# Kernel tuning notes

Hardware: AMD Instinct MI355X
Metric: run time of the kernel (lower is better)

Reference implementation:

```python
import jax, jax.numpy as jnp
from jax import lax
import numpy as np

MS = 128            # local_map_size
HALF = MS // 2
B, S = 8, 64
C, H, W = 3, 1024, 1024


def setup_inputs() -> dict:
    key = jax.random.key(0)
    ks = jax.random.split(key, 48)
    r = lambda i, shape, s: jax.random.normal(ks[i], shape, jnp.float32) * s
    z = lambda *shape: jnp.zeros(shape, jnp.float32)
    o = lambda *shape: jnp.ones(shape, jnp.float32)
    return {
        "full_map": jax.random.normal(ks[0], (B, C, H, W), jnp.float32),
        "conditions": jax.random.uniform(ks[1], (B, 5), jnp.float32, 0.0, 1024.0),
        "input_seq": jax.random.uniform(ks[2], (B, S, 2), jnp.float32, 0.0, 1024.0),
        "steps_remaining": jax.random.uniform(ks[3], (B, S), jnp.float32, 0.0, 500.0),
        # LocalMapEncoder convs (OIHW) + batchnorm affine params
        "cw1": r(4, (16, 3, 3, 3), 0.2),   "cb1": z(16),  "g1": o(16),  "be1": z(16),
        "cw2": r(5, (32, 16, 3, 3), 0.1),  "cb2": z(32),  "g2": o(32),  "be2": z(32),
        "cw3": r(6, (64, 32, 3, 3), 0.07), "cb3": z(64),  "g3": o(64),  "be3": z(64),
        "cw4": r(7, (128, 64, 3, 3), 0.05),"cb4": z(128), "g4": o(128), "be4": z(128),
        "fw1": r(8, (512, 128 * 8 * 8), 0.01), "fb1": z(512),
        "fw2": r(9, (256, 512), 0.04),         "fb2": z(256),
        # ConditionEncoder (6 -> 128 -> 64)
        "ew1": r(10, (128, 6), 0.05),  "eb1": z(128),
        "ew2": r(11, (64, 128), 0.05), "eb2": z(64),
        # coord embedder (2 -> 32)
        "mw": r(12, (32, 2), 0.05), "mb": z(32),
        # 2-layer LSTM, torch gate order (i, f, g, o)
        "w_ih0": r(13, (4 * 256, 32), 0.05),  "w_hh0": r(14, (4 * 256, 256), 0.05),
        "b_ih0": z(4 * 256), "b_hh0": z(4 * 256),
        "w_ih1": r(15, (4 * 256, 256), 0.05), "w_hh1": r(16, (4 * 256, 256), 0.05),
        "b_ih1": z(4 * 256), "b_hh1": z(4 * 256),
        # context layer (256+256+64=576 -> 128 -> 64) and output (64 -> 2)
        "xw1": r(17, (128, 576), 0.04), "xb1": z(128),
        "xw2": r(18, (64, 128), 0.05),  "xb2": z(64),
        "ow": r(19, (2, 64), 0.1),      "ob": z(2),
    }


def _conv_bn_relu(x, w, b, g, be):
    # stride-2 3x3 conv, padding 1, NCHW/OIHW; BatchNorm in training mode (batch stats)
    y = lax.conv_general_dilated(x, w, (2, 2), ((1, 1), (1, 1)),
                                 dimension_numbers=("NCHW", "OIHW", "NCHW"))
    y = y + b[None, :, None, None]
    mu = y.mean((0, 2, 3), keepdims=True)
    var = y.var((0, 2, 3), keepdims=True)
    y = (y - mu) * lax.rsqrt(var + 1e-5) * g[None, :, None, None] + be[None, :, None, None]
    return jax.nn.relu(y)


def _lstm_layer(x, w_ih, w_hh, b_ih, b_hh):
    # x: [B, S, D] -> hidden states [B, S, Hd]
    bsz, hd = x.shape[0], w_hh.shape[1]
    bias = b_ih + b_hh
    def step(carry, xt):
        h, c = carry
        zg = xt @ w_ih.T + h @ w_hh.T + bias
        i, f, gg, oo = jnp.split(zg, 4, axis=-1)
        c = jax.nn.sigmoid(f) * c + jax.nn.sigmoid(i) * jnp.tanh(gg)
        h = jax.nn.sigmoid(oo) * jnp.tanh(c)
        return (h, c), h
    h0 = jnp.zeros((bsz, hd), x.dtype)
    _, hs = lax.scan(step, (h0, h0), x.transpose(1, 0, 2))
    return hs.transpose(1, 0, 2)


def reference(full_map, conditions, input_seq, steps_remaining,
              cw1, cb1, g1, be1, cw2, cb2, g2, be2,
              cw3, cb3, g3, be3, cw4, cb4, g4, be4,
              fw1, fb1, fw2, fb2, ew1, eb1, ew2, eb2, mw, mb,
              w_ih0, w_hh0, b_ih0, b_hh0, w_ih1, w_hh1, b_ih1, b_hh1,
              xw1, xb1, xw2, xb2, ow, ob):
    bsz, seq, _ = input_seq.shape
    # --- batched crop+pad gather (replaces host numpy loop): zero-pad map by
    # HALF on each side, then every crop is a dynamic_slice of size MS at (y, x).
    padded = jnp.pad(full_map, ((0, 0), (0, 0), (HALF, HALF), (HALF, HALF)))
    ys = input_seq[..., 0].astype(jnp.int32).reshape(-1)
    xs = input_seq[..., 1].astype(jnp.int32).reshape(-1)
    bidx = jnp.repeat(jnp.arange(bsz, dtype=jnp.int32), seq)
    crop_one = lambda b, y, x: lax.dynamic_slice(padded, (b, 0, y, x), (1, C, MS, MS))[0]
    crops = jax.vmap(crop_one)(bidx, ys, xs)              # [B*S, C, MS, MS]
    # --- LocalMapEncoder
    h = _conv_bn_relu(crops, cw1, cb1, g1, be1)
    h = _conv_bn_relu(h, cw2, cb2, g2, be2)
    h = _conv_bn_relu(h, cw3, cb3, g3, be3)
    h = _conv_bn_relu(h, cw4, cb4, g4, be4)               # [B*S, 128, 8, 8]
    h = h.reshape(h.shape[0], -1)
    h = jax.nn.relu(h @ fw1.T + fb1) @ fw2.T + fb2
    map_features = h.reshape(bsz, seq, -1)                # [B, S, 256]
    # --- ConditionEncoder on [conditions ++ steps_remaining]
    enh = jnp.concatenate(
        [jnp.broadcast_to(conditions[:, None, :], (bsz, seq, 5)),
         steps_remaining[..., None]], axis=-1)            # [B, S, 6]
    cond_features = jax.nn.relu(enh @ ew1.T + eb1) @ ew2.T + eb2  # [B, S, 64]
    # --- route predictor
    emb = jax.nn.relu(input_seq @ mw.T + mb)              # [B, S, 32]
    lstm_out = _lstm_layer(emb, w_ih0, w_hh0, b_ih0, b_hh0)
    lstm_out = _lstm_layer(lstm_out, w_ih1, w_hh1, b_ih1, b_hh1)  # [B, S, 256]
    combined = jnp.concatenate([lstm_out, map_features, cond_features], axis=-1)
    ctx = jax.nn.relu(jax.nn.relu(combined @ xw1.T + xb1) @ xw2.T + xb2)
    return ctx @ ow.T + ob                                # [B, S, 2]
```

## Files before the change

### kernel.cpp

```cpp
#include <hip/hip_runtime.h>

#define TPB 256
#define NLB 64

typedef float f32x4 __attribute__((ext_vector_type(4)));
typedef short bf16x8 __attribute__((ext_vector_type(8)));
typedef unsigned long long u64;

__device__ __forceinline__ float bf2f(unsigned short u) {
  union { unsigned int i; float f; } x; x.i = ((unsigned int)u) << 16; return x.f;
}
__device__ __forceinline__ unsigned short f2bf(float v) {
  union { float f; unsigned int i; } x; x.f = v;
  unsigned int r = (x.i + 0x7fffu + ((x.i >> 16) & 1u)) >> 16;
  return (unsigned short)r;
}
__device__ __forceinline__ float sigf(float x) { return 1.f / (1.f + __expf(-x)); }
__device__ __forceinline__ bf16x8 lda_bf8(const unsigned short* p) {
  union { uint4 u; bf16x8 v; } t; t.u = *(const uint4*)p; return t.v;
}
__device__ __forceinline__ bf16x8 frag_of(const unsigned int* w) {
  union { unsigned int u[4]; bf16x8 v; } t;
  t.u[0] = w[0]; t.u[1] = w[1]; t.u[2] = w[2]; t.u[3] = w[3]; return t.v;
}

__global__ __launch_bounds__(TPB, 2) void conv1_tap(
    const float* __restrict__ fmap, const float* __restrict__ iseq,
    const unsigned short* __restrict__ wT,
    const float* __restrict__ bias,
    unsigned short* __restrict__ out, float* __restrict__ part) {
  __shared__ __align__(16) unsigned short patch[17][132][8];
  __shared__ unsigned short Bsm[16][104];
  __shared__ float bs[16];
  __shared__ float swsum[4][16], swsq[4][16];
  const int tid = threadIdx.x;
  const int n = blockIdx.x >> 3, R0 = (blockIdx.x & 7) << 3;
  const int y = (int)iseq[n * 2], x = (int)iseq[n * 2 + 1];
  const int bimg = n >> 6;

  for (int e = tid; e < 1536; e += TPB) Bsm[e / 96][e % 96] = wT[e];
  if (tid < 16) bs[tid] = bias[tid];
  for (int e = tid; e < 17 * 132; e += TPB)
    *(uint4*)&patch[e / 132][e % 132][0] = uint4{0u, 0u, 0u, 0u};
  __syncthreads();
  for (int e = tid; e < 3 * 17 * 132; e += TPB) {
    int ic = e / 2244, rem = e % 2244, l = rem / 132, c = rem % 132;
    int i = 2 * R0 - 1 + l, j = c - 1;
    float v = 0.f;
    if ((unsigned)i < 128u && (unsigned)j < 128u) {
      int r = y + i - 64, cc = x + j - 64;
      if ((unsigned)r < 1024u && (unsigned)cc < 1024u)
        v = fmap[(((size_t)bimg * 3 + ic) << 20) + ((size_t)r << 10) + cc];
    }
    patch[l][c][ic] = f2bf(v);
  }
  __syncthreads();

  const int w = tid >> 6, lane = tid & 63, fr = lane & 15, kg = lane >> 4;
  f32x4 acc[8];
#pragma unroll
  for (int m = 0; m < 8; ++m) acc[m] = {0.f, 0.f, 0.f, 0.f};

#pragma unroll
  for (int ch = 0; ch < 3; ++ch) {
    int k8 = ch * 4 + kg;
    int ki = (k8 >= 9) ? 0 : ((k8 * 11) >> 5);
    int kj = (k8 >= 9) ? 0 : (k8 - 3 * ki);
    bf16x8 bfr = lda_bf8(&Bsm[fr][k8 * 8]);
#pragma unroll
    for (int m = 0; m < 8; ++m) {
      int p = w * 128 + m * 16 + fr;
      int pr = p >> 6, pc = p & 63;
      bf16x8 af = lda_bf8(&patch[2 * pr + ki][2 * pc + kj][0]);
      acc[m] = __builtin_amdgcn_mfma_f32_16x16x32_bf16(af, bfr, acc[m], 0, 0, 0);
    }
  }
  const int rg = lane >> 4;
  float bb = bs[fr];
  float sps = 0.f, spq = 0.f;
#pragma unroll
  for (int m = 0; m < 8; ++m) {
#pragma unroll
    for (int r = 0; r < 4; ++r) {
      int p = w * 128 + m * 16 + rg * 4 + r;
      int pr = p >> 6, pc = p & 63;
      float v = acc[m][r] + bb;
      sps += v; spq = fmaf(v, v, spq);
      out[(((size_t)n * 64 + R0 + pr) * 64 + pc) * 16 + fr] = f2bf(v);
    }
  }
  sps += __shfl_xor(sps, 16); spq += __shfl_xor(spq, 16);
  sps += __shfl_xor(sps, 32); spq += __shfl_xor(spq, 32);
  if (lane < 16) { swsum[w][fr] = sps; swsq[w][fr] = spq; }
  __syncthreads();
  if (tid < 16) {
    float s = swsum[0][tid] + swsum[1][tid] + swsum[2][tid] + swsum[3][tid];
    float q = swsq[0][tid] + swsq[1][tid] + swsq[2][tid] + swsq[3][tid];
    part[(size_t)blockIdx.x * 32 + tid * 2] = s;
    part[(size_t)blockIdx.x * 32 + tid * 2 + 1] = q;
  }
}

template<int CIN, int COUT_BLK, int NSPLIT, int HIN, int HOUT>
__global__ __launch_bounds__(TPB, 2) void conv_tap(
    const unsigned short* __restrict__ inb,
    const float* __restrict__ ss,
    const unsigned short* __restrict__ wT,
    const float* __restrict__ bias,
    unsigned short* __restrict__ out, float* __restrict__ part) {
  constexpr int K = CIN * 9;
  constexpr int K8 = K / 8;
  constexpr int NCH = (K8 + 3) / 4;
  constexpr int KPAD = NCH * 32;
  constexpr int BS = KPAD + 8;
  constexpr int CINP = CIN + 8;
  constexpr int ICG_SH = (CIN == 16) ? 1 : (CIN == 32) ? 2 : 3;
  constexpr int TPR = HOUT / 8;
  constexpr int TILES = TPR * TPR;
  constexpr int NT = COUT_BLK / 16;
  constexpr int COUT_TOT = COUT_BLK * NSPLIT;

  __shared__ unsigned short patch[289 * CINP];
  __shared__ unsigned short Bsm[COUT_BLK * BS];
  __shared__ float ssl[CIN * 2];
  __shared__ float swsum[4][COUT_BLK], swsq[4][COUT_BLK];

  const int tid = threadIdx.x;
  const int bid = blockIdx.x;
  const int n = bid / (TILES * NSPLIT);
  const int rem = bid % (TILES * NSPLIT);
  const int tile = rem / NSPLIT;
  const int split = rem % NSPLIT;
  const int TR0 = (tile / TPR) * 8, TC0 = (tile % TPR) * 8;
  const int oc0 = split * COUT_BLK;

  for (int i = tid; i < CIN * 2; i += TPB) ssl[i] = ss[i];
  __syncthreads();

  for (int e = tid; e < 289 * (CIN / 8); e += TPB) {
    int icg = e % (CIN / 8), pix = e / (CIN / 8);
    int row = pix / 17, col = pix % 17;
    int ir = 2 * TR0 - 1 + row, jc = 2 * TC0 - 1 + col;
    uint4 o = {0u, 0u, 0u, 0u};
    if ((unsigned)ir < (unsigned)HIN && (unsigned)jc < (unsigned)HIN) {
      uint4 v = *(const uint4*)&inb[(((size_t)n * HIN + ir) * HIN + jc) * CIN + icg * 8];
      unsigned int d[4] = {v.x, v.y, v.z, v.w};
      unsigned int* op = (unsigned int*)&o;
#pragma unroll
      for (int t = 0; t < 4; ++t) {
        int c = icg * 8 + 2 * t;
        float a = fmaxf(fmaf(bf2f((unsigned short)(d[t] & 0xffff)), ssl[2 * c], ssl[2 * c + 1]), 0.f);
        float b = fmaxf(fmaf(bf2f((unsigned short)(d[t] >> 16)), ssl[2 * c + 2], ssl[2 * c + 3]), 0.f);
        op[t] = (unsigned int)f2bf(a) | ((unsigned int)f2bf(b) << 16);
      }
    }
    *(uint4*)&patch[pix * CINP + icg * 8] = o;
  }
  constexpr int B8 = COUT_BLK * (KPAD / 8);
  for (int e = tid; e < B8; e += TPB) {
    int oc = e / (KPAD / 8), k8i = e % (KPAD / 8);
    uint4 v = {0u, 0u, 0u, 0u};
    if (k8i * 8 < K) v = *(const uint4*)&wT[(size_t)(oc0 + oc) * K + k8i * 8];
    *(uint4*)&Bsm[oc * BS + k8i * 8] = v;
  }
  __syncthreads();

  const int wave = tid >> 6, lane = tid & 63;
  const int fr = lane & 15, kg = lane >> 4;
  const int p = wave * 16 + fr;
  const int pr = p >> 3, pc = p & 7;
  f32x4 acc[NT];
#pragma unroll
  for (int j = 0; j < NT; ++j) acc[j] = {0.f, 0.f, 0.f, 0.f};

#pragma unroll
  for (int ch = 0; ch < NCH; ++ch) {
    int k8 = ch * 4 + kg;
    int tap = k8 >> ICG_SH, icg = k8 & ((1 << ICG_SH) - 1);
    int ki = (tap * 11) >> 5;
    int kj = tap - 3 * ki;
    int addr = ((2 * pr + ki) * 17 + (2 * pc + kj)) * CINP + icg * 8;
    if (tap >= 9) addr = 0;
    bf16x8 af = lda_bf8(&patch[addr]);
#pragma unroll
    for (int j = 0; j < NT; ++j) {
      bf16x8 bfr = lda_bf8(&Bsm[(j * 16 + fr) * BS + ch * 32 + kg * 8]);
      acc[j] = __builtin_amdgcn_mfma_f32_16x16x32_bf16(af, bfr, acc[j], 0, 0, 0);
    }
  }
  const int rg = lane >> 4;
#pragma unroll
  for (int j = 0; j < NT; ++j) {
    int oc = oc0 + j * 16 + fr;
    float bb = bias[oc];
    float s1 = 0.f, q1 = 0.f;
#pragma unroll
    for (int r = 0; r < 4; ++r) {
      int pp = wave * 16 + rg * 4 + r;
      int orow = TR0 + (pp >> 3), ocol = TC0 + (pp & 7);
      float v = acc[j][r] + bb;
      s1 += v; q1 = fmaf(v, v, q1);
      out[(((size_t)n * HOUT + orow) * HOUT + ocol) * COUT_TOT + oc] = f2bf(v);
    }
    s1 += __shfl_xor(s1, 16); q1 += __shfl_xor(q1, 16);
    s1 += __shfl_xor(s1, 32); q1 += __shfl_xor(q1, 32);
    if (lane < 16) { swsum[wave][j * 16 + fr] = s1; swsq[wave][j * 16 + fr] = q1; }
  }
  __syncthreads();
  if (tid < COUT_BLK) {
    float s = swsum[0][tid] + swsum[1][tid] + swsum[2][tid] + swsum[3][tid];
    float q = swsq[0][tid] + swsq[1][tid] + swsq[2][tid] + swsq[3][tid];
    part[(size_t)bid * COUT_BLK * 2 + tid * 2] = s;
    part[(size_t)bid * COUT_BLK * 2 + tid * 2 + 1] = q;
  }
}

__global__ __launch_bounds__(TPB) void stats_final3(const float* __restrict__ part,
    const float* __restrict__ gamma, const float* __restrict__ beta,
    float* __restrict__ ss, float inv_count, int COUT_BLK, int NSPLIT, int NBID) {
  const int c = blockIdx.x, tid = threadIdx.x;
  const int split = c / COUT_BLK, loc = c % COUT_BLK;
  const int NG = NBID / NSPLIT;
  float s = 0.f, q = 0.f;
  for (int g = tid; g < NG; g += TPB) {
    size_t b = (size_t)g * NSPLIT + split;
    s += part[b * COUT_BLK * 2 + loc * 2];
    q += part[b * COUT_BLK * 2 + loc * 2 + 1];
  }
  __shared__ float rs[TPB], rq[TPB];
  rs[tid] = s; rq[tid] = q;
  __syncthreads();
  for (int off = TPB / 2; off > 0; off >>= 1) {
    if (tid < off) { rs[tid] += rs[tid + off]; rq[tid] += rq[tid + off]; }
    __syncthreads();
  }
  if (tid == 0) {
    float mean = rs[0] * inv_count;
    float var  = rq[0] * inv_count - mean * mean;
    float rstd = rsqrtf(var + 1e-5f);
    float scl  = gamma[c] * rstd;
    ss[2 * c] = scl;
    ss[2 * c + 1] = beta[c] - mean * scl;
  }
}

__global__ __launch_bounds__(TPB) void prep_wt(
    const float* __restrict__ w1, const float* __restrict__ w2,
    const float* __restrict__ w3, const float* __restrict__ w4,
    unsigned short* __restrict__ wt1, unsigned short* __restrict__ wt2,
    unsigned short* __restrict__ wt3, unsigned short* __restrict__ wt4) {
  int i = blockIdx.x * TPB + threadIdx.x;
  if (i < 1536) {
    int oc = i / 96, k = i % 96;
    int tap = k >> 3, ic = k & 7;
    float v = (tap < 9 && ic < 3) ? w1[(oc * 3 + ic) * 9 + tap] : 0.f;
    wt1[i] = f2bf(v);
  } else if (i < 6144) {
    int j = i - 1536;
    int oc = j / 144, k = j % 144;
    wt2[j] = f2bf(w2[(oc * 16 + (k & 15)) * 9 + (k >> 4)]);
  } else if (i < 24576) {
    int j = i - 6144;
    int oc = j / 288, k = j % 288;
    wt3[j] = f2bf(w3[(oc * 32 + (k & 31)) * 9 + (k >> 5)]);
  } else if (i < 98304) {
    int j = i - 24576;
    int oc = j / 576, k = j % 576;
    wt4[j] = f2bf(w4[(oc * 64 + (k & 63)) * 9 + (k >> 6)]);
  }
}

__global__ __launch_bounds__(TPB) void permute_fw1(const float* __restrict__ in,
    unsigned short* __restrict__ out) {
  __shared__ unsigned short l[128 * 66];
  int n = blockIdx.x;
  for (int e = threadIdx.x; e < 8192; e += TPB) {
    int c = e >> 6, pix = e & 63;
    l[c * 66 + pix] = f2bf(in[(size_t)n * 8192 + e]);
  }
  __syncthreads();
  for (int e = threadIdx.x; e < 8192; e += TPB) {
    int pix = e >> 7, c = e & 127;
    out[(size_t)n * 8192 + e] = l[c * 66 + pix];
  }
}

__device__ __forceinline__ uint4 bnpack(uint4 v, const float* sst) {
  unsigned int d[4] = {v.x, v.y, v.z, v.w};
  uint4 o; unsigned int* op = (unsigned int*)&o;
#pragma unroll
  for (int t = 0; t < 4; ++t) {
    float a = fmaxf(fmaf(bf2f((unsigned short)(d[t] & 0xffff)), sst[4 * t], sst[4 * t + 1]), 0.f);
    float b = fmaxf(fmaf(bf2f((unsigned short)(d[t] >> 16)), sst[4 * t + 2], sst[4 * t + 3]), 0.f);
    op[t] = (unsigned int)f2bf(a) | ((unsigned int)f2bf(b) << 16);
  }
  return o;
}

__global__ __launch_bounds__(TPB, 2) void fc1_mfma(
    const unsigned short* __restrict__ A, const unsigned short* __restrict__ W,
    const float* __restrict__ ss, const float* __restrict__ bias,
    float* __restrict__ out) {
  __shared__ unsigned short As[64][64];
  __shared__ unsigned short Bs[64][64];
  __shared__ float ssl[256];
  const int tid = threadIdx.x;
  const int lane = tid & 63, wave = tid >> 6;
  const int wr = (wave >> 1) * 32, wc = (wave & 1) * 32;
  const int bm = blockIdx.y * 64, bn = blockIdx.x * 64;
  f32x4 acc00 = {0.f, 0.f, 0.f, 0.f}, acc01 = acc00, acc10 = acc00, acc11 = acc00;
  const int r0 = tid >> 3, c0 = tid & 7;
  const int fr = lane & 15, kg = lane >> 4;
  for (int i = tid; i < 256; i += TPB) ssl[i] = ss[i];
  __syncthreads();
  for (int kt = 0; kt < 128; ++kt) {
    const int kb = kt * 64;
    uint4 av0 = *(const uint4*)&A[(size_t)(bm + r0) * 8192 + kb + c0 * 8];
    uint4 av1 = *(const uint4*)&A[(size_t)(bm + r0 + 32) * 8192 + kb + c0 * 8];
    uint4 bv0 = *(const uint4*)&W[(size_t)(bn + r0) * 8192 + kb + c0 * 8];
    uint4 bv1 = *(const uint4*)&W[(size_t)(bn + r0 + 32) * 8192 + kb + c0 * 8];
    const float* sst = &ssl[2 * ((kb + c0 * 8) & 127)];
    __syncthreads();
    av0 = bnpack(av0, sst);
    av1 = bnpack(av1, sst);
    *(uint4*)&As[r0][(c0 ^ (r0 & 7)) * 8] = av0;
    *(uint4*)&As[r0 + 32][(c0 ^ (r0 & 7)) * 8] = av1;
    *(uint4*)&Bs[r0][(c0 ^ (r0 & 7)) * 8] = bv0;
    *(uint4*)&Bs[r0 + 32][(c0 ^ (r0 & 7)) * 8] = bv1;
    __syncthreads();
#pragma unroll
    for (int ks = 0; ks < 2; ++ks) {
      int ch = ks * 4 + kg;
      int ra0 = wr + fr, ra1 = wr + 16 + fr;
      int rb0 = wc + fr, rb1 = wc + 16 + fr;
      bf16x8 a_0 = lda_bf8(&As[ra0][(ch ^ (ra0 & 7)) * 8]);
      bf16x8 a_1 = lda_bf8(&As[ra1][(ch ^ (ra1 & 7)) * 8]);
      bf16x8 b_0 = lda_bf8(&Bs[rb0][(ch ^ (rb0 & 7)) * 8]);
      bf16x8 b_1 = lda_bf8(&Bs[rb1][(ch ^ (rb1 & 7)) * 8]);
      acc00 = __builtin_amdgcn_mfma_f32_16x16x32_bf16(a_0, b_0, acc00, 0, 0, 0);
      acc01 = __builtin_amdgcn_mfma_f32_16x16x32_bf16(a_0, b_1, acc01, 0, 0, 0);
      acc10 = __builtin_amdgcn_mfma_f32_16x16x32_bf16(a_1, b_0, acc10, 0, 0, 0);
      acc11 = __builtin_amdgcn_mfma_f32_16x16x32_bf16(a_1, b_1, acc11, 0, 0, 0);
    }
  }
  const int rg = lane >> 4;
  int n0 = bn + wc + fr, n1 = n0 + 16;
  float bi0 = bias[n0], bi1 = bias[n1];
#pragma unroll
  for (int r = 0; r < 4; ++r) {
    int m0 = bm + wr + rg * 4 + r, m1 = m0 + 16;
    out[m0 * 512 + n0] = fmaxf(acc00[r] + bi0, 0.f);
    out[m0 * 512 + n1] = fmaxf(acc01[r] + bi1, 0.f);
    out[m1 * 512 + n0] = fmaxf(acc10[r] + bi0, 0.f);
    out[m1 * 512 + n1] = fmaxf(acc11[r] + bi1, 0.f);
  }
}

__global__ __launch_bounds__(TPB, 2) void gemm_m64(
    const float* __restrict__ A, const float* __restrict__ W,
    const float* __restrict__ bias, float* __restrict__ out,
    int N, int K, int relu, int ldo, int coff) {
  __shared__ unsigned short As[64 * 40];
  __shared__ unsigned short Bs[64 * 40];
  const int tid = threadIdx.x, lane = tid & 63, wave = tid >> 6;
  const int wr = (wave >> 1) * 32, wc = (wave & 1) * 32;
  const int bm = blockIdx.y * 64, bn = blockIdx.x * 64;
  const int fr = lane & 15, kg = lane >> 4;
  const int sr = tid >> 2, sc = (tid & 3) * 8;
  f32x4 a00 = {0.f, 0.f, 0.f, 0.f}, a01 = a00, a10 = a00, a11 = a00;
  int nch = (K + 31) >> 5;
  for (int ch = 0; ch < nch; ++ch) {
    int kb = ch * 32;
    __syncthreads();
    {
      unsigned short tmp[8];
#pragma unroll
      for (int j = 0; j < 8; ++j) {
        int k = kb + sc + j;
        tmp[j] = (k < K) ? f2bf(A[(size_t)(bm + sr) * K + k]) : (unsigned short)0;
      }
      *(uint4*)&As[sr * 40 + sc] = *(const uint4*)tmp;
      int wrow = bn + sr;
#pragma unroll
      for (int j = 0; j < 8; ++j) {
        int k = kb + sc + j;
        tmp[j] = (wrow < N && k < K) ? f2bf(W[(size_t)wrow * K + k]) : (unsigned short)0;
      }
      *(uint4*)&Bs[sr * 40 + sc] = *(const uint4*)tmp;
    }
    __syncthreads();
    bf16x8 af0 = lda_bf8(&As[(wr + fr) * 40 + kg * 8]);
    bf16x8 af1 = lda_bf8(&As[(wr + 16 + fr) * 40 + kg * 8]);
    bf16x8 bf0 = lda_bf8(&Bs[(wc + fr) * 40 + kg * 8]);
    bf16x8 bf1 = lda_bf8(&Bs[(wc + 16 + fr) * 40 + kg * 8]);
    a00 = __builtin_amdgcn_mfma_f32_16x16x32_bf16(af0, bf0, a00, 0, 0, 0);
    a01 = __builtin_amdgcn_mfma_f32_16x16x32_bf16(af0, bf1, a01, 0, 0, 0);
    a10 = __builtin_amdgcn_mfma_f32_16x16x32_bf16(af1, bf0, a10, 0, 0, 0);
    a11 = __builtin_amdgcn_mfma_f32_16x16x32_bf16(af1, bf1, a11, 0, 0, 0);
  }
  const int rg = lane >> 4;
  int n0 = bn + wc + fr, n1 = n0 + 16;
  float bi0 = (n0 < N) ? bias[n0] : 0.f;
  float bi1 = (n1 < N) ? bias[n1] : 0.f;
#pragma unroll
  for (int r = 0; r < 4; ++r) {
    int m0 = bm + wr + rg * 4 + r, m1 = m0 + 16;
    if (n0 < N) {
      float v = a00[r] + bi0; out[(size_t)m0 * ldo + coff + n0] = relu ? fmaxf(v, 0.f) : v;
      v = a10[r] + bi0;       out[(size_t)m1 * ldo + coff + n0] = relu ? fmaxf(v, 0.f) : v;
    }
    if (n1 < N) {
      float v = a01[r] + bi1; out[(size_t)m0 * ldo + coff + n1] = relu ? fmaxf(v, 0.f) : v;
      v = a11[r] + bi1;       out[(size_t)m1 * ldo + coff + n1] = relu ? fmaxf(v, 0.f) : v;
    }
  }
}

__global__ __launch_bounds__(TPB) void cond_enc(
    const float* __restrict__ cond, const float* __restrict__ steps,
    const float* __restrict__ ew1, const float* __restrict__ eb1,
    const float* __restrict__ ew2, const float* __restrict__ eb2,
    float* __restrict__ comb) {
  __shared__ float w1s[128][8];
  __shared__ float w2s[64][132];
  __shared__ float hbuf[64][132];
  const int tid = threadIdx.x;
  const int row0 = blockIdx.x * 64;
  for (int e = tid; e < 128 * 8; e += TPB) {
    int k = e >> 3, t = e & 7;
    w1s[k][t] = (t < 6) ? ew1[k * 6 + t] : (t == 6 ? eb1[k] : 0.f);
  }
  for (int e = tid; e < 64 * 128; e += TPB) {
    int j = e >> 7, k = e & 127;
    w2s[j][k] = ew2[j * 128 + k];
  }
  __syncthreads();
  {
    int row = tid >> 2, ks = tid & 3;
    int n = row0 + row;
    int b = n >> 6, s = n & 63;
    float e0 = cond[b * 5], e1 = cond[b * 5 + 1], e2 = cond[b * 5 + 2];
    float e3 = cond[b * 5 + 3], e4 = cond[b * 5 + 4];
    float e5 = steps[b * 64 + s];
    for (int k = ks * 32; k < ks * 32 + 32; ++k) {
      float a = fmaf(w1s[k][0], e0, fmaf(w1s[k][1], e1, fmaf(w1s[k][2], e2,
                fmaf(w1s[k][3], e3, fmaf(w1s[k][4], e4, fmaf(w1s[k][5], e5, w1s[k][6]))))));
      hbuf[row][k] = fmaxf(a, 0.f);
    }
  }
  __syncthreads();
  {
    int row = tid >> 2, js = tid & 3;
    int n = row0 + row;
    for (int j = js * 16; j < js * 16 + 16; ++j) {
      float a = eb2[j];
#pragma unroll 8
      for (int k = 0; k < 128; ++k) a = fmaf(w2s[j][k], hbuf[row][k], a);
      comb[(size_t)n * 576 + 512 + j] = a;
    }
  }
}

__global__ __launch_bounds__(TPB, 1) void lstm_kernel(
    const float* __restrict__ iseq,
    const float* __restrict__ mw, const float* __restrict__ mb,
    const float* __restrict__ w_ih0, const float* __restrict__ w_hh0,
    const float* __restrict__ b_ih0, const float* __restrict__ b_hh0,
    const float* __restrict__ w_ih1, const float* __restrict__ w_hh1,
    const float* __restrict__ b_ih1, const float* __restrict__ b_hh1,
    u64* __restrict__ h0x, u64* __restrict__ h1x,
    float* __restrict__ comb) {
  const int tid = threadIdx.x;
  const int blkid = blockIdx.x;
  const int u0 = blkid * 4;

  __shared__ float xz[64][8][16];
  __shared__ __align__(16) char reg2[18944];
  __shared__ float bias1s[16];

  float (*embc)[8][32] = (float (*)[8][32])reg2;
  float* mwmb = (float*)(reg2 + 16384);
  unsigned short (*v0s)[264] = (unsigned short (*)[264])reg2;
  unsigned short (*w1h)[264] = (unsigned short (*)[264])(reg2 + 8448);
  float (*P0)[16]  = (float (*)[16])(reg2 + 16896);
  float (*P1a)[16] = (float (*)[16])(reg2 + 17408);
  float (*P1b)[16] = (float (*)[16])(reg2 + 17920);

  const int wv = tid >> 6, lane = tid & 63, fr = lane & 15, kg = lane >> 4;
  const int r = tid & 15, ks = tid >> 4;
  const int R  = (r >> 2) * 256 + u0 + (r & 3);
  const int Rf = (fr >> 2) * 256 + u0 + (fr & 3);

  unsigned int wfrag[8][4];
  {
    const float* wsrc = (wv == 0) ? w_hh0 : (wv == 1) ? w_ih1 : w_hh1;
#pragma unroll
    for (int ch = 0; ch < 8; ++ch)
#pragma unroll
      for (int d = 0; d < 4; ++d) {
        float lo = wsrc[(size_t)Rf * 256 + ch * 32 + kg * 8 + d * 2];
        float hi = wsrc[(size_t)Rf * 256 + ch * 32 + kg * 8 + d * 2 + 1];
        wfrag[ch][d] = (unsigned)f2bf(lo) | ((unsigned)f2bf(hi) << 16);
      }
  }
  float wtmp[32];
#pragma unroll
  for (int i = 0; i < 32; ++i) wtmp[i] = w_ih0[R * 32 + i];
  const float bias0r = b_ih0[R] + b_hh0[R];
  if (tid < 16) bias1s[tid] = b_ih1[R] + b_hh1[R];
  if (tid < 96) mwmb[tid] = (tid < 64) ? mw[tid] : mb[tid - 64];
  __syncthreads();

  for (int chunk = 0; chunk < 4; ++chunk) {
    if (tid < 128) {
      int pp = tid >> 3, b = tid & 7;
      int pg = chunk * 16 + pp;
      float s0 = iseq[(b * 64 + pg) * 2 + 0];
      float s1 = iseq[(b * 64 + pg) * 2 + 1];
      for (int k = 0; k < 32; ++k)
        embc[pp][b][k] = fmaxf(fmaf(mwmb[2 * k], s0, fmaf(mwmb[2 * k + 1], s1, mwmb[64 + k])), 0.f);
    }
    __syncthreads();
    {
      int pg = chunk * 16 + ks;
      for (int b = 0; b < 8; ++b) {
        float a = bias0r;
        const float* e = &embc[ks][b][0];
#pragma unroll
        for (int k = 0; k < 32; ++k) a = fmaf(wtmp[k], e[k], a);
        xz[pg][b][r] = a;
      }
    }
    __syncthreads();
  }

  for (int i = tid; i < 8 * 264; i += TPB) {
    v0s[8 + i / 264][i % 264] = 0;
    w1h[8 + i / 264][i % 264] = 0;
  }
  __syncthreads();

  float c0 = 0.f, c1 = 0.f;
  for (int p = 0; p <= 64; ++p) {
    if (tid < 128) {
      if (p >= 1) {
        const unsigned tag0 = (unsigned)p;
        const u64* s0p = &h0x[(size_t)(p - 1) * 1024 + tid * 8];
        u64 e[8];
        for (;;) {
          bool ok = true;
#pragma unroll
          for (int i = 0; i < 8; ++i) {
            e[i] = __hip_atomic_load(&s0p[i], __ATOMIC_RELAXED, __HIP_MEMORY_SCOPE_AGENT);
            ok &= ((unsigned)(e[i] >> 32) == tag0);
          }
          if (ok) break;
          __builtin_amdgcn_s_sleep(1);
        }
#pragma unroll
        for (int i = 0; i < 8; ++i) {
          int g = tid * 8 + i;
          int bb = (g >> 1) & 7, ub = (g >> 4) * 4 + (g & 1) * 2;
          *(unsigned int*)&v0s[bb][ub] = (unsigned int)e[i];
        }
      } else {
#pragma unroll
        for (int i = 0; i < 8; ++i) {
          int g = tid * 8 + i;
          int bb = (g >> 1) & 7, ub = (g >> 4) * 4 + (g & 1) * 2;
          *(unsigned int*)&v0s[bb][ub] = 0u;
        }
      }
    } else {
      int t2 = tid - 128;
      if (p >= 2) {
        const unsigned tag1 = (unsigned)(p - 1);
        const u64* s1p = &h1x[(size_t)(p - 2) * 1024 + t2 * 8];
        u64 e[8];
        for (;;) {
          bool ok = true;
#pragma unroll
          for (int i = 0; i < 8; ++i) {
            e[i] = __hip_atomic_load(&s1p[i], __ATOMIC_RELAXED, __HIP_MEMORY_SCOPE_AGENT);
            ok &= ((unsigned)(e[i] >> 32) == tag1);
          }
          if (ok) break;
          __builtin_amdgcn_s_sleep(1);
        }
#pragma unroll
        for (int i = 0; i < 8; ++i) {
          int g = t2 * 8 + i;
          int bb = (g >> 1) & 7, ub = (g >> 4) * 4 + (g & 1) * 2;
          *(unsigned int*)&w1h[bb][ub] = (unsigned int)e[i];
        }
      } else {
#pragma unroll
        for (int i = 0; i < 8; ++i) {
          int g = t2 * 8 + i;
          int bb = (g >> 1) & 7, ub = (g >> 4) * 4 + (g & 1) * 2;
          *(unsigned int*)&w1h[bb][ub] = 0u;
        }
      }
    }
    __syncthreads();

    if (wv == 0) {
      if (p < 64) {
        f32x4 acc = {0.f, 0.f, 0.f, 0.f};
#pragma unroll
        for (int ch = 0; ch < 8; ++ch) {
          bf16x8 af = lda_bf8(&v0s[fr][ch * 32 + kg * 8]);
          acc = __builtin_amdgcn_mfma_f32_16x16x32_bf16(af, frag_of(wfrag[ch]), acc, 0, 0, 0);
        }
#pragma unroll
        for (int j = 0; j < 4; ++j) {
          int bb2 = (lane >> 4) * 4 + j;
          if (bb2 < 8) P0[bb2][fr] = acc[j];
        }
      }
    } else if (wv == 1) {
      if (p >= 1) {
        f32x4 acc = {0.f, 0.f, 0.f, 0.f};
#pragma unroll
        for (int ch = 0; ch < 8; ++ch) {
          bf16x8 af = lda_bf8(&v0s[fr][ch * 32 + kg * 8]);
          acc = __builtin_amdgcn_mfma_f32_16x16x32_bf16(af, frag_of(wfrag[ch]), acc, 0, 0, 0);
        }
#pragma unroll
        for (int j = 0; j < 4; ++j) {
          int bb2 = (lane >> 4) * 4 + j;
          if (bb2 < 8) P1a[bb2][fr] = acc[j];
        }
      }
    } else if (wv == 2) {
      if (p >= 1) {
        f32x4 acc = {0.f, 0.f, 0.f, 0.f};
#pragma unroll
        for (int ch = 0; ch < 8; ++ch) {
          bf16x8 af = lda_bf8(&w1h[fr][ch * 32 + kg * 8]);
          acc = __builtin_amdgcn_mfma_f32_16x16x32_bf16(af, frag_of(wfrag[ch]), acc, 0, 0, 0);
        }
#pragma unroll
        for (int j = 0; j < 4; ++j) {
          int bb2 = (lane >> 4) * 4 + j;
          if (bb2 < 8) P1b[bb2][fr] = acc[j];
        }
      }
    }
    __syncthreads();

    if (tid < 32 && p < 64) {
      int b = tid >> 2, uu = tid & 3;
      float zi = P0[b][uu]      + xz[p][b][uu];
      float zf = P0[b][4 + uu]  + xz[p][b][4 + uu];
      float zg = P0[b][8 + uu]  + xz[p][b][8 + uu];
      float zo = P0[b][12 + uu] + xz[p][b][12 + uu];
      c0 = sigf(zf) * c0 + sigf(zi) * tanhf(zg);
      float h = sigf(zo) * tanhf(c0);
      float hp = __shfl_xor(h, 1);
      if (!(uu & 1)) {
        unsigned int d = (unsigned int)f2bf(h) | ((unsigned int)f2bf(hp) << 16);
        u64 v = ((u64)(unsigned)(p + 1) << 32) | d;
        __hip_atomic_store(&h0x[(size_t)p * 1024 + blkid * 16 + b * 2 + (uu >> 1)], v,
                           __ATOMIC_RELAXED, __HIP_MEMORY_SCOPE_AGENT);
      }
    } else if (tid >= 32 && tid < 64 && p >= 1) {
      int t2 = tid - 32, b = t2 >> 2, uu = t2 & 3;
      float zi = P1a[b][uu]      + P1b[b][uu]      + bias1s[uu];
      float zf = P1a[b][4 + uu]  + P1b[b][4 + uu]  + bias1s[4 + uu];
      float zg = P1a[b][8 + uu]  + P1b[b][8 + uu]  + bias1s[8 + uu];
      float zo = P1a[b][12 + uu] + P1b[b][12 + uu] + bias1s[12 + uu];
      c1 = sigf(zf) * c1 + sigf(zi) * tanhf(zg);
      float h = sigf(zo) * tanhf(c1);
      comb[(size_t)(b * 64 + (p - 1)) * 576 + u0 + uu] = h;
      float hp = __shfl_xor(h, 1);
      if (!(uu & 1)) {
        unsigned int d = (unsigned int)f2bf(h) | ((unsigned int)f2bf(hp) << 16);
        u64 v = ((u64)(unsigned)p << 32) | d;
        __hip_atomic_store(&h1x[(size_t)(p - 1) * 1024 + blkid * 16 + b * 2 + (uu >> 1)], v,
                           __ATOMIC_RELAXED, __HIP_MEMORY_SCOPE_AGENT);
      }
    }
  }
}

extern "C" void kernel_launch(void* const* d_in, const int* in_sizes, int n_in,
                              void* d_out, int out_size, void* d_ws, size_t ws_size,
                              hipStream_t stream) {
  const float* fmap  = (const float*)d_in[0];
  const float* cond  = (const float*)d_in[1];
  const float* iseq  = (const float*)d_in[2];
  const float* steps = (const float*)d_in[3];
  const float* cw1 = (const float*)d_in[4];  const float* cb1 = (const float*)d_in[5];
  const float* g1  = (const float*)d_in[6];  const float* be1 = (const float*)d_in[7];
  const float* cw2 = (const float*)d_in[8];  const float* cb2 = (const float*)d_in[9];
  const float* g2  = (const float*)d_in[10]; const float* be2 = (const float*)d_in[11];
  const float* cw3 = (const float*)d_in[12]; const float* cb3 = (const float*)d_in[13];
  const float* g3  = (const float*)d_in[14]; const float* be3 = (const float*)d_in[15];
  const float* cw4 = (const float*)d_in[16]; const float* cb4 = (const float*)d_in[17];
  const float* g4  = (const float*)d_in[18]; const float* be4 = (const float*)d_in[19];
  const float* fw1 = (const float*)d_in[20]; const float* fb1 = (const float*)d_in[21];
  const float* fw2 = (const float*)d_in[22]; const float* fb2 = (const float*)d_in[23];
  const float* ew1 = (const float*)d_in[24]; const float* eb1 = (const float*)d_in[25];
  const float* ew2 = (const float*)d_in[26]; const float* eb2 = (const float*)d_in[27];
  const float* mw  = (const float*)d_in[28]; const float* mb  = (const float*)d_in[29];
  const float* w_ih0 = (const float*)d_in[30]; const float* w_hh0 = (const float*)d_in[31];
  const float* b_ih0 = (const float*)d_in[32]; const float* b_hh0 = (const float*)d_in[33];
  const float* w_ih1 = (const float*)d_in[34]; const float* w_hh1 = (const float*)d_in[35];
  const float* b_ih1 = (const float*)d_in[36]; const float* b_hh1 = (const float*)d_in[37];
  const float* xw1 = (const float*)d_in[38]; const float* xb1 = (const float*)d_in[39];
  const float* xw2 = (const float*)d_in[40]; const float* xb2 = (const float*)d_in[41];
  const float* ow  = (const float*)d_in[42]; const float* ob  = (const float*)d_in[43];

  float* ws = (float*)d_ws;
  unsigned short* y1bf  = (unsigned short*)ws;
  unsigned short* y2bf  = (unsigned short*)(ws + 16777216);
  unsigned short* y3bf  = (unsigned short*)(ws + 25165824);
  unsigned short* y4pre = (unsigned short*)(ws + 29360128);
  unsigned short* fw1bf = (unsigned short*)(ws + 33554432);
  size_t base = 35651584;
  float* part  = ws + base; base += 524288;
  float* ss1   = ws + base; base += 32;
  float* ss2   = ws + base; base += 64;
  float* ss3   = ws + base; base += 128;
  float* ss4   = ws + base; base += 256;
  float* f1    = ws + base; base += 262144;
  u64*   h0x   = (u64*)(ws + base); base += 131072;
  u64*   h1x   = (u64*)(ws + base); base += 131072;
  float* comb  = ws + base; base += 294912;
  float* cx1   = ws + base; base += 65536;
  float* cx2   = ws + base; base += 32768;
  unsigned short* wt1 = (unsigned short*)(ws + base); base += 768;
  unsigned short* wt2 = (unsigned short*)(ws + base); base += 2304;
  unsigned short* wt3 = (unsigned short*)(ws + base); base += 9216;
  unsigned short* wt4 = (unsigned short*)(ws + base); base += 36864;

  prep_wt<<<384, TPB, 0, stream>>>(cw1, cw2, cw3, cw4, wt1, wt2, wt3, wt4);
  permute_fw1<<<512, TPB, 0, stream>>>(fw1, fw1bf);

  conv1_tap<<<4096, TPB, 0, stream>>>(fmap, iseq, wt1, cb1, y1bf, part);
  stats_final3<<<16, TPB, 0, stream>>>(part, g1, be1, ss1, 1.f / 2097152.f, 16, 1, 4096);
  conv_tap<16, 32, 1, 64, 32><<<8192, TPB, 0, stream>>>(y1bf, ss1, wt2, cb2, y2bf, part);
  stats_final3<<<32, TPB, 0, stream>>>(part, g2, be2, ss2, 1.f / 524288.f, 32, 1, 8192);
  conv_tap<32, 64, 1, 32, 16><<<2048, TPB, 0, stream>>>(y2bf, ss2, wt3, cb3, y3bf, part);
  stats_final3<<<64, TPB, 0, stream>>>(part, g3, be3, ss3, 1.f / 131072.f, 64, 1, 2048);
  conv_tap<64, 32, 4, 16, 8><<<2048, TPB, 0, stream>>>(y3bf, ss3, wt4, cb4, y4pre, part);
  stats_final3<<<128, TPB, 0, stream>>>(part, g4, be4, ss4, 1.f / 32768.f, 32, 4, 2048);

  hipMemsetAsync(h0x, 0, 2 * 64 * 1024 * sizeof(u64), stream);
  lstm_kernel<<<NLB, TPB, 0, stream>>>(iseq, mw, mb,
                                       w_ih0, w_hh0, b_ih0, b_hh0,
                                       w_ih1, w_hh1, b_ih1, b_hh1,
                                       h0x, h1x, comb);

  fc1_mfma<<<dim3(8, 8), TPB, 0, stream>>>(y4pre, fw1bf, ss4, fb1, f1);
  gemm_m64<<<dim3(4, 8), TPB, 0, stream>>>(f1, fw2, fb2, comb, 256, 512, 0, 576, 256);

  cond_enc<<<8, TPB, 0, stream>>>(cond, steps, ew1, eb1, ew2, eb2, comb);

  gemm_m64<<<dim3(2, 8), TPB, 0, stream>>>(comb, xw1, xb1, cx1, 128, 576, 1, 128, 0);
  gemm_m64<<<dim3(1, 8), TPB, 0, stream>>>(cx1, xw2, xb2, cx2, 64, 128, 1, 64, 0);
  gemm_m64<<<dim3(1, 8), TPB, 0, stream>>>(cx2, ow, ob, (float*)d_out, 2, 64, 0, 2, 0);
}
```

Before: 675.5 us.

## Split LSTM recurrence into segments co-scheduled with conv and fc1 kernels

The serial 64-step LSTM kernel is split into step segments. Each segment runs in the first 64 blocks of the conv1, conv2-4 and fc1 launches, so the latency-bound recurrence overlaps with the bandwidth-heavy encoder convolutions. Cell state and the input projection are saved to and restored from workspace between segments, and the per-segment weight fragments are reloaded each time. This relies on the 64 LSTM blocks being resident together, since they spin-wait on each other. It also adds shared-memory pressure and a reload cost for every segment.

```diff
diff --git a/kernel.cpp b/kernel.cpp
--- a/kernel.cpp
+++ b/kernel.cpp
@@ -23,18 +23,280 @@
   union { unsigned int u[4]; bf16x8 v; } t;
   t.u[0] = w[0]; t.u[1] = w[1]; t.u[2] = w[2]; t.u[3] = w[3]; return t.v;
 }
-
-__global__ __launch_bounds__(TPB, 2) void conv1_tap(
+__device__ __forceinline__ uint4 bnpack(uint4 v, const float* sst) {
+  unsigned int d[4] = {v.x, v.y, v.z, v.w};
+  uint4 o; unsigned int* op = (unsigned int*)&o;
+#pragma unroll
+  for (int t = 0; t < 4; ++t) {
+    float a = fmaxf(fmaf(bf2f((unsigned short)(d[t] & 0xffff)), sst[4 * t], sst[4 * t + 1]), 0.f);
+    float b = fmaxf(fmaf(bf2f((unsigned short)(d[t] >> 16)), sst[4 * t + 2], sst[4 * t + 3]), 0.f);
+    op[t] = (unsigned int)f2bf(a) | ((unsigned int)f2bf(b) << 16);
+  }
+  return o;
+}
+
+__device__ void lstm_seg(int blkid, int p0, int p1, int first,
+    const float* __restrict__ iseq, const float* __restrict__ mw, const float* __restrict__ mb,
+    const float* __restrict__ w_ih0, const float* __restrict__ w_hh0,
+    const float* __restrict__ b_ih0, const float* __restrict__ b_hh0,
+    const float* __restrict__ w_ih1, const float* __restrict__ w_hh1,
+    const float* __restrict__ b_ih1, const float* __restrict__ b_hh1,
+    u64* __restrict__ h0x, u64* __restrict__ h1x,
+    float* __restrict__ comb, float* __restrict__ xzg, float* __restrict__ cst,
+    char* sm) {
+  const int tid = threadIdx.x;
+  const int u0 = blkid * 4;
+  float (*xz)[8][16] = (float (*)[8][16])sm;
+  char* reg2 = sm + 32768;
+  float* bias1s = (float*)(sm + 51712);
+
+  float (*embc)[8][32] = (float (*)[8][32])reg2;
+  float* mwmb = (float*)(reg2 + 16384);
+  unsigned short (*v0s)[264] = (unsigned short (*)[264])reg2;
+  unsigned short (*w1h)[264] = (unsigned short (*)[264])(reg2 + 8448);
+  float (*P0)[16]  = (float (*)[16])(reg2 + 16896);
+  float (*P1a)[16] = (float (*)[16])(reg2 + 17408);
+  float (*P1b)[16] = (float (*)[16])(reg2 + 17920);
+
+  const int wv = tid >> 6, lane = tid & 63, fr = lane & 15, kg = lane >> 4;
+  const int r = tid & 15, ks = tid >> 4;
+  const int R  = (r >> 2) * 256 + u0 + (r & 3);
+  const int Rf = (fr >> 2) * 256 + u0 + (fr & 3);
+
+  unsigned int wfrag[8][4];
+  {
+    const float* wsrc = (wv == 0) ? w_hh0 : (wv == 1) ? w_ih1 : w_hh1;
+#pragma unroll
+    for (int ch = 0; ch < 8; ++ch)
+#pragma unroll
+      for (int d = 0; d < 4; ++d) {
+        float lo = wsrc[(size_t)Rf * 256 + ch * 32 + kg * 8 + d * 2];
+        float hi = wsrc[(size_t)Rf * 256 + ch * 32 + kg * 8 + d * 2 + 1];
+        wfrag[ch][d] = (unsigned)f2bf(lo) | ((unsigned)f2bf(hi) << 16);
+      }
+  }
+  if (tid < 16) bias1s[tid] = b_ih1[R] + b_hh1[R];
+
+  if (first) {
+    float wtmp[32];
+#pragma unroll
+    for (int i = 0; i < 32; ++i) wtmp[i] = w_ih0[R * 32 + i];
+    const float bias0r = b_ih0[R] + b_hh0[R];
+    if (tid < 96) mwmb[tid] = (tid < 64) ? mw[tid] : mb[tid - 64];
+    __syncthreads();
+    for (int chunk = 0; chunk < 4; ++chunk) {
+      if (tid < 128) {
+        int pp = tid >> 3, b = tid & 7;
+        int pg = chunk * 16 + pp;
+        float s0 = iseq[(b * 64 + pg) * 2 + 0];
+        float s1 = iseq[(b * 64 + pg) * 2 + 1];
+        for (int k = 0; k < 32; ++k)
+          embc[pp][b][k] = fmaxf(fmaf(mwmb[2 * k], s0, fmaf(mwmb[2 * k + 1], s1, mwmb[64 + k])), 0.f);
+      }
+      __syncthreads();
+      {
+        int pg = chunk * 16 + ks;
+        for (int b = 0; b < 8; ++b) {
+          float a = bias0r;
+          const float* e = &embc[ks][b][0];
+#pragma unroll
+          for (int k = 0; k < 32; ++k) a = fmaf(wtmp[k], e[k], a);
+          xz[pg][b][r] = a;
+        }
+      }
+      __syncthreads();
+    }
+    for (int i = tid; i < 8192; i += TPB)
+      xzg[(size_t)blkid * 8192 + i] = ((float*)xz)[i];
+  } else {
+    __syncthreads();
+    for (int i = tid; i < 8192; i += TPB)
+      ((float*)xz)[i] = xzg[(size_t)blkid * 8192 + i];
+  }
+  __syncthreads();
+
+  for (int i = tid; i < 8 * 264; i += TPB) {
+    v0s[8 + i / 264][i % 264] = 0;
+    w1h[8 + i / 264][i % 264] = 0;
+  }
+  float c0 = 0.f, c1 = 0.f;
+  if (!first) {
+    if (tid < 32) c0 = cst[blkid * 64 + tid];
+    else if (tid < 64) c1 = cst[blkid * 64 + tid];
+  }
+  __syncthreads();
+
+  for (int p = p0; p < p1; ++p) {
+    if (tid < 128) {
+      if (p >= 1) {
+        const unsigned tag0 = (unsigned)p;
+        const u64* s0p = &h0x[(size_t)(p - 1) * 1024 + tid * 8];
+        u64 e[8];
+        for (;;) {
+          bool ok = true;
+#pragma unroll
+          for (int i = 0; i < 8; ++i) {
+            e[i] = __hip_atomic_load(&s0p[i], __ATOMIC_RELAXED, __HIP_MEMORY_SCOPE_AGENT);
+            ok &= ((unsigned)(e[i] >> 32) == tag0);
+          }
+          if (ok) break;
+          __builtin_amdgcn_s_sleep(1);
+        }
+#pragma unroll
+        for (int i = 0; i < 8; ++i) {
+          int g = tid * 8 + i;
+          int bb = (g >> 1) & 7, ub = (g >> 4) * 4 + (g & 1) * 2;
+          *(unsigned int*)&v0s[bb][ub] = (unsigned int)e[i];
+        }
+      } else {
+#pragma unroll
+        for (int i = 0; i < 8; ++i) {
+          int g = tid * 8 + i;
+          int bb = (g >> 1) & 7, ub = (g >> 4) * 4 + (g & 1) * 2;
+          *(unsigned int*)&v0s[bb][ub] = 0u;
+        }
+      }
+    } else {
+      int t2 = tid - 128;
+      if (p >= 2) {
+        const unsigned tag1 = (unsigned)(p - 1);
+        const u64* s1p = &h1x[(size_t)(p - 2) * 1024 + t2 * 8];
+        u64 e[8];
+        for (;;) {
+          bool ok = true;
+#pragma unroll
+          for (int i = 0; i < 8; ++i) {
+            e[i] = __hip_atomic_load(&s1p[i], __ATOMIC_RELAXED, __HIP_MEMORY_SCOPE_AGENT);
+            ok &= ((unsigned)(e[i] >> 32) == tag1);
+          }
+          if (ok) break;
+          __builtin_amdgcn_s_sleep(1);
+        }
+#pragma unroll
+        for (int i = 0; i < 8; ++i) {
+          int g = t2 * 8 + i;
+          int bb = (g >> 1) & 7, ub = (g >> 4) * 4 + (g & 1) * 2;
+          *(unsigned int*)&w1h[bb][ub] = (unsigned int)e[i];
+        }
+      } else {
+#pragma unroll
+        for (int i = 0; i < 8; ++i) {
+          int g = t2 * 8 + i;
+          int bb = (g >> 1) & 7, ub = (g >> 4) * 4 + (g & 1) * 2;
+          *(unsigned int*)&w1h[bb][ub] = 0u;
+        }
+      }
+    }
+    __syncthreads();
+
+    if (wv == 0) {
+      if (p < 64) {
+        f32x4 acc = {0.f, 0.f, 0.f, 0.f};
+#pragma unroll
+        for (int ch = 0; ch < 8; ++ch) {
+          bf16x8 af = lda_bf8(&v0s[fr][ch * 32 + kg * 8]);
+          acc = __builtin_amdgcn_mfma_f32_16x16x32_bf16(af, frag_of(wfrag[ch]), acc, 0, 0, 0);
+        }
+#pragma unroll
+        for (int j = 0; j < 4; ++j) {
+          int bb2 = (lane >> 4) * 4 + j;
+          if (bb2 < 8) P0[bb2][fr] = acc[j];
+        }
+      }
+    } else if (wv == 1) {
+      if (p >= 1) {
+        f32x4 acc = {0.f, 0.f, 0.f, 0.f};
+#pragma unroll
+        for (int ch = 0; ch < 8; ++ch) {
+          bf16x8 af = lda_bf8(&v0s[fr][ch * 32 + kg * 8]);
+          acc = __builtin_amdgcn_mfma_f32_16x16x32_bf16(af, frag_of(wfrag[ch]), acc, 0, 0, 0);
+        }
+#pragma unroll
+        for (int j = 0; j < 4; ++j) {
+          int bb2 = (lane >> 4) * 4 + j;
+          if (bb2 < 8) P1a[bb2][fr] = acc[j];
+        }
+      }
+    } else if (wv == 2) {
+      if (p >= 1) {
+        f32x4 acc = {0.f, 0.f, 0.f, 0.f};
+#pragma unroll
+        for (int ch = 0; ch < 8; ++ch) {
+          bf16x8 af = lda_bf8(&w1h[fr][ch * 32 + kg * 8]);
+          acc = __builtin_amdgcn_mfma_f32_16x16x32_bf16(af, frag_of(wfrag[ch]), acc, 0, 0, 0);
+        }
+#pragma unroll
+        for (int j = 0; j < 4; ++j) {
+          int bb2 = (lane >> 4) * 4 + j;
+          if (bb2 < 8) P1b[bb2][fr] = acc[j];
+        }
+      }
+    }
+    __syncthreads();
+
+    if (tid < 32 && p < 64) {
+      int b = tid >> 2, uu = tid & 3;
+      float zi = P0[b][uu]      + xz[p][b][uu];
+      float zf = P0[b][4 + uu]  + xz[p][b][4 + uu];
+      float zg = P0[b][8 + uu]  + xz[p][b][8 + uu];
+      float zo = P0[b][12 + uu] + xz[p][b][12 + uu];
+      c0 = sigf(zf) * c0 + sigf(zi) * tanhf(zg);
+      float h = sigf(zo) * tanhf(c0);
+      float hp = __shfl_xor(h, 1);
+      if (!(uu & 1)) {
+        unsigned int d = (unsigned int)f2bf(h) | ((unsigned int)f2bf(hp) << 16);
+        u64 v = ((u64)(unsigned)(p + 1) << 32) | d;
+        __hip_atomic_store(&h0x[(size_t)p * 1024 + blkid * 16 + b * 2 + (uu >> 1)], v,
+                           __ATOMIC_RELAXED, __HIP_MEMORY_SCOPE_AGENT);
+      }
+    } else if (tid >= 32 && tid < 64 && p >= 1) {
+      int t2 = tid - 32, b = t2 >> 2, uu = t2 & 3;
+      float zi = P1a[b][uu]      + P1b[b][uu]      + bias1s[uu];
+      float zf = P1a[b][4 + uu]  + P1b[b][4 + uu]  + bias1s[4 + uu];
+      float zg = P1a[b][8 + uu]  + P1b[b][8 + uu]  + bias1s[8 + uu];
+      float zo = P1a[b][12 + uu] + P1b[b][12 + uu] + bias1s[12 + uu];
+      c1 = sigf(zf) * c1 + sigf(zi) * tanhf(zg);
+      float h = sigf(zo) * tanhf(c1);
+      comb[(size_t)(b * 64 + (p - 1)) * 576 + u0 + uu] = h;
+      float hp = __shfl_xor(h, 1);
+      if (!(uu & 1)) {
+        unsigned int d = (unsigned int)f2bf(h) | ((unsigned int)f2bf(hp) << 16);
+        u64 v = ((u64)(unsigned)p << 32) | d;
+        __hip_atomic_store(&h1x[(size_t)(p - 1) * 1024 + blkid * 16 + b * 2 + (uu >> 1)], v,
+                           __ATOMIC_RELAXED, __HIP_MEMORY_SCOPE_AGENT);
+      }
+    }
+  }
+
+  if (tid < 32) cst[blkid * 64 + tid] = c0;
+  else if (tid < 64) cst[blkid * 64 + tid] = c1;
+}
+
+#define LSTM_ARGS const float* __restrict__ iseq_l, const float* __restrict__ mw, const float* __restrict__ mb, \
+    const float* __restrict__ w_ih0, const float* __restrict__ w_hh0, \
+    const float* __restrict__ b_ih0, const float* __restrict__ b_hh0, \
+    const float* __restrict__ w_ih1, const float* __restrict__ w_hh1, \
+    const float* __restrict__ b_ih1, const float* __restrict__ b_hh1, \
+    u64* __restrict__ h0x, u64* __restrict__ h1x, float* __restrict__ comb, \
+    float* __restrict__ xzg, float* __restrict__ cst, int p0, int p1, int first
+#define LSTM_PASS(blk) lstm_seg(blk, p0, p1, first, iseq_l, mw, mb, w_ih0, w_hh0, b_ih0, b_hh0, \
+    w_ih1, w_hh1, b_ih1, b_hh1, h0x, h1x, comb, xzg, cst, sm)
+
+__global__ __launch_bounds__(TPB, 2) void k_conv1(
     const float* __restrict__ fmap, const float* __restrict__ iseq,
-    const unsigned short* __restrict__ wT,
-    const float* __restrict__ bias,
-    unsigned short* __restrict__ out, float* __restrict__ part) {
-  __shared__ __align__(16) unsigned short patch[17][132][8];
-  __shared__ unsigned short Bsm[16][104];
-  __shared__ float bs[16];
-  __shared__ float swsum[4][16], swsq[4][16];
+    const unsigned short* __restrict__ wT, const float* __restrict__ bias,
+    unsigned short* __restrict__ out, float* __restrict__ part, LSTM_ARGS) {
+  __shared__ __align__(16) char sm[52288];
   const int tid = threadIdx.x;
-  const int n = blockIdx.x >> 3, R0 = (blockIdx.x & 7) << 3;
+  if (blockIdx.x < NLB) { LSTM_PASS(blockIdx.x); return; }
+  const int bidc = blockIdx.x - NLB;
+  unsigned short (*patch)[132][8] = (unsigned short (*)[132][8])sm;
+  unsigned short (*Bsm)[104] = (unsigned short (*)[104])(sm + 35904);
+  float* bs = (float*)(sm + 39232);
+  float* swsum = (float*)(sm + 39296);
+  float* swsq  = (float*)(sm + 39552);
+
+  const int n = bidc >> 3, R0 = (bidc & 7) << 3;
   const int y = (int)iseq[n * 2], x = (int)iseq[n * 2 + 1];
   const int bimg = n >> 6;
 
@@ -60,7 +322,6 @@
   f32x4 acc[8];
 #pragma unroll
   for (int m = 0; m < 8; ++m) acc[m] = {0.f, 0.f, 0.f, 0.f};
-
 #pragma unroll
   for (int ch = 0; ch < 3; ++ch) {
     int k8 = ch * 4 + kg;
@@ -91,23 +352,21 @@
   }
   sps += __shfl_xor(sps, 16); spq += __shfl_xor(spq, 16);
   sps += __shfl_xor(sps, 32); spq += __shfl_xor(spq, 32);
-  if (lane < 16) { swsum[w][fr] = sps; swsq[w][fr] = spq; }
+  if (lane < 16) { swsum[w * 16 + fr] = sps; swsq[w * 16 + fr] = spq; }
   __syncthreads();
   if (tid < 16) {
-    float s = swsum[0][tid] + swsum[1][tid] + swsum[2][tid] + swsum[3][tid];
-    float q = swsq[0][tid] + swsq[1][tid] + swsq[2][tid] + swsq[3][tid];
-    part[(size_t)blockIdx.x * 32 + tid * 2] = s;
-    part[(size_t)blockIdx.x * 32 + tid * 2 + 1] = q;
-  }
-}
-
-template<int CIN, int COUT_BLK, int NSPLIT, int HIN, int HOUT>
-__global__ __launch_bounds__(TPB, 2) void conv_tap(
-    const unsigned short* __restrict__ inb,
-    const float* __restrict__ ss,
-    const unsigned short* __restrict__ wT,
-    const float* __restrict__ bias,
-    unsigned short* __restrict__ out, float* __restrict__ part) {
+    float s = swsum[tid] + swsum[16 + tid] + swsum[32 + tid] + swsum[48 + tid];
+    float q = swsq[tid] + swsq[16 + tid] + swsq[32 + tid] + swsq[48 + tid];
+    part[(size_t)bidc * 32 + tid * 2] = s;
+    part[(size_t)bidc * 32 + tid * 2 + 1] = q;
+  }
+}
+
+template<int CIN, int CB, int NS, int HIN, int HOUT>
+__global__ __launch_bounds__(TPB, 2) void k_conv(
+    const unsigned short* __restrict__ inb, const float* __restrict__ ssx,
+    const unsigned short* __restrict__ wT, const float* __restrict__ bias,
+    unsigned short* __restrict__ out, float* __restrict__ part, LSTM_ARGS) {
   constexpr int K = CIN * 9;
   constexpr int K8 = K / 8;
   constexpr int NCH = (K8 + 3) / 4;
@@ -116,25 +375,31 @@
   constexpr int CINP = CIN + 8;
   constexpr int ICG_SH = (CIN == 16) ? 1 : (CIN == 32) ? 2 : 3;
   constexpr int TPR = HOUT / 8;
-  constexpr int TILES = TPR * TPR;
-  constexpr int NT = COUT_BLK / 16;
-  constexpr int COUT_TOT = COUT_BLK * NSPLIT;
-
-  __shared__ unsigned short patch[289 * CINP];
-  __shared__ unsigned short Bsm[COUT_BLK * BS];
-  __shared__ float ssl[CIN * 2];
-  __shared__ float swsum[4][COUT_BLK], swsq[4][COUT_BLK];
-
+  constexpr int NT = CB / 16;
+  constexpr int COUT_TOT = CB * NS;
+  constexpr int PB = 289 * CINP * 2;
+  constexpr int BB = CB * BS * 2;
+  constexpr int CONVSM = PB + BB + CIN * 8 + CB * 32;
+  constexpr int SMSZ = CONVSM > 52288 ? CONVSM : 52288;
+  __shared__ __align__(16) char sm[SMSZ];
   const int tid = threadIdx.x;
-  const int bid = blockIdx.x;
-  const int n = bid / (TILES * NSPLIT);
-  const int rem = bid % (TILES * NSPLIT);
-  const int tile = rem / NSPLIT;
-  const int split = rem % NSPLIT;
+  if (blockIdx.x < NLB) { LSTM_PASS(blockIdx.x); return; }
+  const int bidc = blockIdx.x - NLB;
+
+  unsigned short* patch = (unsigned short*)sm;
+  unsigned short* Bsm = (unsigned short*)(sm + PB);
+  float* ssl = (float*)(sm + PB + BB);
+  float* swsum = (float*)(sm + PB + BB + CIN * 8);
+  float* swsq = swsum + 4 * CB;
+
+  const int n = bidc / ((TPR * TPR) * NS);
+  const int rem = bidc % ((TPR * TPR) * NS);
+  const int tile = rem / NS;
+  const int split = rem % NS;
   const int TR0 = (tile / TPR) * 8, TC0 = (tile % TPR) * 8;
-  const int oc0 = split * COUT_BLK;
-
-  for (int i = tid; i < CIN * 2; i += TPB) ssl[i] = ss[i];
+  const int oc0 = split * CB;
+
+  for (int i = tid; i < CIN * 2; i += TPB) ssl[i] = ssx[i];
   __syncthreads();
 
   for (int e = tid; e < 289 * (CIN / 8); e += TPB) {
@@ -156,8 +421,7 @@
     }
     *(uint4*)&patch[pix * CINP + icg * 8] = o;
   }
-  constexpr int B8 = COUT_BLK * (KPAD / 8);
-  for (int e = tid; e < B8; e += TPB) {
+  for (int e = tid; e < CB * (KPAD / 8); e += TPB) {
     int oc = e / (KPAD / 8), k8i = e % (KPAD / 8);
     uint4 v = {0u, 0u, 0u, 0u};
     if (k8i * 8 < K) v = *(const uint4*)&wT[(size_t)(oc0 + oc) * K + k8i * 8];
@@ -204,14 +468,77 @@
     }
     s1 += __shfl_xor(s1, 16); q1 += __shfl_xor(q1, 16);
     s1 += __shfl_xor(s1, 32); q1 += __shfl_xor(q1, 32);
-    if (lane < 16) { swsum[wave][j * 16 + fr] = s1; swsq[wave][j * 16 + fr] = q1; }
-  }
-  __syncthreads();
-  if (tid < COUT_BLK) {
-    float s = swsum[0][tid] + swsum[1][tid] + swsum[2][tid] + swsum[3][tid];
-    float q = swsq[0][tid] + swsq[1][tid] + swsq[2][tid] + swsq[3][tid];
-    part[(size_t)bid * COUT_BLK * 2 + tid * 2] = s;
-    part[(size_t)bid * COUT_BLK * 2 + tid * 2 + 1] = q;
+    if (lane < 16) { swsum[wave * CB + j * 16 + fr] = s1; swsq[wave * CB + j * 16 + fr] = q1; }
+  }
+  __syncthreads();
+  if (tid < CB) {
+    float s = swsum[tid] + swsum[CB + tid] + swsum[2 * CB + tid] + swsum[3 * CB + tid];
+    float q = swsq[tid] + swsq[CB + tid] + swsq[2 * CB + tid] + swsq[3 * CB + tid];
+    part[(size_t)bidc * CB * 2 + tid * 2] = s;
+    part[(size_t)bidc * CB * 2 + tid * 2 + 1] = q;
+  }
+}
+
+__global__ __launch_bounds__(TPB, 2) void k_fc1(
+    const unsigned short* __restrict__ A, const unsigned short* __restrict__ W,
+    const float* __restrict__ ssx, const float* __restrict__ bias, float* __restrict__ out,
+    LSTM_ARGS) {
+  __shared__ __align__(16) char sm[52288];
+  const int tid = threadIdx.x;
+  if (blockIdx.x < NLB) { LSTM_PASS(blockIdx.x); return; }
+  const int cid = blockIdx.x - NLB;
+  const int bm = (cid >> 3) * 64, bn = (cid & 7) * 64;
+
+  unsigned short (*As)[64] = (unsigned short (*)[64])sm;
+  unsigned short (*Bs)[64] = (unsigned short (*)[64])(sm + 8192);
+  float* ssl = (float*)(sm + 16384);
+  const int lane = tid & 63, wave = tid >> 6;
+  const int wr = (wave >> 1) * 32, wc = (wave & 1) * 32;
+  f32x4 acc00 = {0.f, 0.f, 0.f, 0.f}, acc01 = acc00, acc10 = acc00, acc11 = acc00;
+  const int r0 = tid >> 3, c0 = tid & 7;
+  const int fr = lane & 15, kg = lane >> 4;
+  for (int i = tid; i < 256; i += TPB) ssl[i] = ssx[i];
+  __syncthreads();
+  for (int kt = 0; kt < 128; ++kt) {
+    const int kb = kt * 64;
+    uint4 av0 = *(const uint4*)&A[(size_t)(bm + r0) * 8192 + kb + c0 * 8];
+    uint4 av1 = *(const uint4*)&A[(size_t)(bm + r0 + 32) * 8192 + kb + c0 * 8];
+    uint4 bv0 = *(const uint4*)&W[(size_t)(bn + r0) * 8192 + kb + c0 * 8];
+    uint4 bv1 = *(const uint4*)&W[(size_t)(bn + r0 + 32) * 8192 + kb + c0 * 8];
+    const float* sst = &ssl[2 * ((kb + c0 * 8) & 127)];
+    __syncthreads();
+    av0 = bnpack(av0, sst);
+    av1 = bnpack(av1, sst);
+    *(uint4*)&As[r0][(c0 ^ (r0 & 7)) * 8] = av0;
+    *(uint4*)&As[r0 + 32][(c0 ^ (r0 & 7)) * 8] = av1;
+    *(uint4*)&Bs[r0][(c0 ^ (r0 & 7)) * 8] = bv0;
+    *(uint4*)&Bs[r0 + 32][(c0 ^ (r0 & 7)) * 8] = bv1;
+    __syncthreads();
+#pragma unroll
+    for (int ks = 0; ks < 2; ++ks) {
+      int ch = ks * 4 + kg;
+      int ra0 = wr + fr, ra1 = wr + 16 + fr;
+      int rb0 = wc + fr, rb1 = wc + 16 + fr;
+      bf16x8 a_0 = lda_bf8(&As[ra0][(ch ^ (ra0 & 7)) * 8]);
+      bf16x8 a_1 = lda_bf8(&As[ra1][(ch ^ (ra1 & 7)) * 8]);
+      bf16x8 b_0 = lda_bf8(&Bs[rb0][(ch ^ (rb0 & 7)) * 8]);
+      bf16x8 b_1 = lda_bf8(&Bs[rb1][(ch ^ (rb1 & 7)) * 8]);
+      acc00 = __builtin_amdgcn_mfma_f32_16x16x32_bf16(a_0, b_0, acc00, 0, 0, 0);
+      acc01 = __builtin_amdgcn_mfma_f32_16x16x32_bf16(a_0, b_1, acc01, 0, 0, 0);
+      acc10 = __builtin_amdgcn_mfma_f32_16x16x32_bf16(a_1, b_0, acc10, 0, 0, 0);
+      acc11 = __builtin_amdgcn_mfma_f32_16x16x32_bf16(a_1, b_1, acc11, 0, 0, 0);
+    }
+  }
+  const int rg = lane >> 4;
+  int n0 = bn + wc + fr, n1 = n0 + 16;
+  float bi0 = bias[n0], bi1 = bias[n1];
+#pragma unroll
+  for (int r = 0; r < 4; ++r) {
+    int m0 = bm + wr + rg * 4 + r, m1 = m0 + 16;
+    out[m0 * 512 + n0] = fmaxf(acc00[r] + bi0, 0.f);
+    out[m0 * 512 + n1] = fmaxf(acc01[r] + bi1, 0.f);
+    out[m1 * 512 + n0] = fmaxf(acc10[r] + bi0, 0.f);
+    out[m1 * 512 + n1] = fmaxf(acc11[r] + bi1, 0.f);
   }
 }
 
@@ -285,77 +612,6 @@
   }
 }
 
-__device__ __forceinline__ uint4 bnpack(uint4 v, const float* sst) {
-  unsigned int d[4] = {v.x, v.y, v.z, v.w};
-  uint4 o; unsigned int* op = (unsigned int*)&o;
-#pragma unroll
-  for (int t = 0; t < 4; ++t) {
-    float a = fmaxf(fmaf(bf2f((unsigned short)(d[t] & 0xffff)), sst[4 * t], sst[4 * t + 1]), 0.f);
-    float b = fmaxf(fmaf(bf2f((unsigned short)(d[t] >> 16)), sst[4 * t + 2], sst[4 * t + 3]), 0.f);
-    op[t] = (unsigned int)f2bf(a) | ((unsigned int)f2bf(b) << 16);
-  }
-  return o;
-}
-
-__global__ __launch_bounds__(TPB, 2) void fc1_mfma(
-    const unsigned short* __restrict__ A, const unsigned short* __restrict__ W,
-    const float* __restrict__ ss, const float* __restrict__ bias,
-    float* __restrict__ out) {
-  __shared__ unsigned short As[64][64];
-  __shared__ unsigned short Bs[64][64];
-  __shared__ float ssl[256];
-  const int tid = threadIdx.x;
-  const int lane = tid & 63, wave = tid >> 6;
-  const int wr = (wave >> 1) * 32, wc = (wave & 1) * 32;
-  const int bm = blockIdx.y * 64, bn = blockIdx.x * 64;
-  f32x4 acc00 = {0.f, 0.f, 0.f, 0.f}, acc01 = acc00, acc10 = acc00, acc11 = acc00;
-  const int r0 = tid >> 3, c0 = tid & 7;
-  const int fr = lane & 15, kg = lane >> 4;
-  for (int i = tid; i < 256; i += TPB) ssl[i] = ss[i];
-  __syncthreads();
-  for (int kt = 0; kt < 128; ++kt) {
-    const int kb = kt * 64;
-    uint4 av0 = *(const uint4*)&A[(size_t)(bm + r0) * 8192 + kb + c0 * 8];
-    uint4 av1 = *(const uint4*)&A[(size_t)(bm + r0 + 32) * 8192 + kb + c0 * 8];
-    uint4 bv0 = *(const uint4*)&W[(size_t)(bn + r0) * 8192 + kb + c0 * 8];
-    uint4 bv1 = *(const uint4*)&W[(size_t)(bn + r0 + 32) * 8192 + kb + c0 * 8];
-    const float* sst = &ssl[2 * ((kb + c0 * 8) & 127)];
-    __syncthreads();
-    av0 = bnpack(av0, sst);
-    av1 = bnpack(av1, sst);
-    *(uint4*)&As[r0][(c0 ^ (r0 & 7)) * 8] = av0;
-    *(uint4*)&As[r0 + 32][(c0 ^ (r0 & 7)) * 8] = av1;
-    *(uint4*)&Bs[r0][(c0 ^ (r0 & 7)) * 8] = bv0;
-    *(uint4*)&Bs[r0 + 32][(c0 ^ (r0 & 7)) * 8] = bv1;
-    __syncthreads();
-#pragma unroll
-    for (int ks = 0; ks < 2; ++ks) {
-      int ch = ks * 4 + kg;
-      int ra0 = wr + fr, ra1 = wr + 16 + fr;
-      int rb0 = wc + fr, rb1 = wc + 16 + fr;
-      bf16x8 a_0 = lda_bf8(&As[ra0][(ch ^ (ra0 & 7)) * 8]);
-      bf16x8 a_1 = lda_bf8(&As[ra1][(ch ^ (ra1 & 7)) * 8]);
-      bf16x8 b_0 = lda_bf8(&Bs[rb0][(ch ^ (rb0 & 7)) * 8]);
-      bf16x8 b_1 = lda_bf8(&Bs[rb1][(ch ^ (rb1 & 7)) * 8]);
-      acc00 = __builtin_amdgcn_mfma_f32_16x16x32_bf16(a_0, b_0, acc00, 0, 0, 0);
-      acc01 = __builtin_amdgcn_mfma_f32_16x16x32_bf16(a_0, b_1, acc01, 0, 0, 0);
-      acc10 = __builtin_amdgcn_mfma_f32_16x16x32_bf16(a_1, b_0, acc10, 0, 0, 0);
-      acc11 = __builtin_amdgcn_mfma_f32_16x16x32_bf16(a_1, b_1, acc11, 0, 0, 0);
-    }
-  }
-  const int rg = lane >> 4;
-  int n0 = bn + wc + fr, n1 = n0 + 16;
-  float bi0 = bias[n0], bi1 = bias[n1];
-#pragma unroll
-  for (int r = 0; r < 4; ++r) {
-    int m0 = bm + wr + rg * 4 + r, m1 = m0 + 16;
-    out[m0 * 512 + n0] = fmaxf(acc00[r] + bi0, 0.f);
-    out[m0 * 512 + n1] = fmaxf(acc01[r] + bi1, 0.f);
-    out[m1 * 512 + n0] = fmaxf(acc10[r] + bi0, 0.f);
-    out[m1 * 512 + n1] = fmaxf(acc11[r] + bi1, 0.f);
-  }
-}
-
 __global__ __launch_bounds__(TPB, 2) void gemm_m64(
     const float* __restrict__ A, const float* __restrict__ W,
     const float* __restrict__ bias, float* __restrict__ out,
@@ -457,229 +713,6 @@
 #pragma unroll 8
       for (int k = 0; k < 128; ++k) a = fmaf(w2s[j][k], hbuf[row][k], a);
       comb[(size_t)n * 576 + 512 + j] = a;
-    }
-  }
-}
-
-__global__ __launch_bounds__(TPB, 1) void lstm_kernel(
-    const float* __restrict__ iseq,
-    const float* __restrict__ mw, const float* __restrict__ mb,
-    const float* __restrict__ w_ih0, const float* __restrict__ w_hh0,
-    const float* __restrict__ b_ih0, const float* __restrict__ b_hh0,
-    const float* __restrict__ w_ih1, const float* __restrict__ w_hh1,
-    const float* __restrict__ b_ih1, const float* __restrict__ b_hh1,
-    u64* __restrict__ h0x, u64* __restrict__ h1x,
-    float* __restrict__ comb) {
-  const int tid = threadIdx.x;
-  const int blkid = blockIdx.x;
-  const int u0 = blkid * 4;
-
-  __shared__ float xz[64][8][16];
-  __shared__ __align__(16) char reg2[18944];
-  __shared__ float bias1s[16];
-
-  float (*embc)[8][32] = (float (*)[8][32])reg2;
-  float* mwmb = (float*)(reg2 + 16384);
-  unsigned short (*v0s)[264] = (unsigned short (*)[264])reg2;
-  unsigned short (*w1h)[264] = (unsigned short (*)[264])(reg2 + 8448);
-  float (*P0)[16]  = (float (*)[16])(reg2 + 16896);
-  float (*P1a)[16] = (float (*)[16])(reg2 + 17408);
-  float (*P1b)[16] = (float (*)[16])(reg2 + 17920);
-
-  const int wv = tid >> 6, lane = tid & 63, fr = lane & 15, kg = lane >> 4;
-  const int r = tid & 15, ks = tid >> 4;
-  const int R  = (r >> 2) * 256 + u0 + (r & 3);
-  const int Rf = (fr >> 2) * 256 + u0 + (fr & 3);
-
-  unsigned int wfrag[8][4];
-  {
-    const float* wsrc = (wv == 0) ? w_hh0 : (wv == 1) ? w_ih1 : w_hh1;
-#pragma unroll
-    for (int ch = 0; ch < 8; ++ch)
-#pragma unroll
-      for (int d = 0; d < 4; ++d) {
-        float lo = wsrc[(size_t)Rf * 256 + ch * 32 + kg * 8 + d * 2];
-        float hi = wsrc[(size_t)Rf * 256 + ch * 32 + kg * 8 + d * 2 + 1];
-        wfrag[ch][d] = (unsigned)f2bf(lo) | ((unsigned)f2bf(hi) << 16);
-      }
-  }
-  float wtmp[32];
-#pragma unroll
-  for (int i = 0; i < 32; ++i) wtmp[i] = w_ih0[R * 32 + i];
-  const float bias0r = b_ih0[R] + b_hh0[R];
-  if (tid < 16) bias1s[tid] = b_ih1[R] + b_hh1[R];
-  if (tid < 96) mwmb[tid] = (tid < 64) ? mw[tid] : mb[tid - 64];
-  __syncthreads();
-
-  for (int chunk = 0; chunk < 4; ++chunk) {
-    if (tid < 128) {
-      int pp = tid >> 3, b = tid & 7;
-      int pg = chunk * 16 + pp;
-      float s0 = iseq[(b * 64 + pg) * 2 + 0];
-      float s1 = iseq[(b * 64 + pg) * 2 + 1];
-      for (int k = 0; k < 32; ++k)
-        embc[pp][b][k] = fmaxf(fmaf(mwmb[2 * k], s0, fmaf(mwmb[2 * k + 1], s1, mwmb[64 + k])), 0.f);
-    }
-    __syncthreads();
-    {
-      int pg = chunk * 16 + ks;
-      for (int b = 0; b < 8; ++b) {
-        float a = bias0r;
-        const float* e = &embc[ks][b][0];
-#pragma unroll
-        for (int k = 0; k < 32; ++k) a = fmaf(wtmp[k], e[k], a);
-        xz[pg][b][r] = a;
-      }
-    }
-    __syncthreads();
-  }
-
-  for (int i = tid; i < 8 * 264; i += TPB) {
-    v0s[8 + i / 264][i % 264] = 0;
-    w1h[8 + i / 264][i % 264] = 0;
-  }
-  __syncthreads();
-
-  float c0 = 0.f, c1 = 0.f;
-  for (int p = 0; p <= 64; ++p) {
-    if (tid < 128) {
-      if (p >= 1) {
-        const unsigned tag0 = (unsigned)p;
-        const u64* s0p = &h0x[(size_t)(p - 1) * 1024 + tid * 8];
-        u64 e[8];
-        for (;;) {
-          bool ok = true;
-#pragma unroll
-          for (int i = 0; i < 8; ++i) {
-            e[i] = __hip_atomic_load(&s0p[i], __ATOMIC_RELAXED, __HIP_MEMORY_SCOPE_AGENT);
-            ok &= ((unsigned)(e[i] >> 32) == tag0);
-          }
-          if (ok) break;
-          __builtin_amdgcn_s_sleep(1);
-        }
-#pragma unroll
-        for (int i = 0; i < 8; ++i) {
-          int g = tid * 8 + i;
-          int bb = (g >> 1) & 7, ub = (g >> 4) * 4 + (g & 1) * 2;
-          *(unsigned int*)&v0s[bb][ub] = (unsigned int)e[i];
-        }
-      } else {
-#pragma unroll
-        for (int i = 0; i < 8; ++i) {
-          int g = tid * 8 + i;
-          int bb = (g >> 1) & 7, ub = (g >> 4) * 4 + (g & 1) * 2;
-          *(unsigned int*)&v0s[bb][ub] = 0u;
-        }
-      }
-    } else {
-      int t2 = tid - 128;
-      if (p >= 2) {
-        const unsigned tag1 = (unsigned)(p - 1);
-        const u64* s1p = &h1x[(size_t)(p - 2) * 1024 + t2 * 8];
-        u64 e[8];
-        for (;;) {
-          bool ok = true;
-#pragma unroll
-          for (int i = 0; i < 8; ++i) {
-            e[i] = __hip_atomic_load(&s1p[i], __ATOMIC_RELAXED, __HIP_MEMORY_SCOPE_AGENT);
-            ok &= ((unsigned)(e[i] >> 32) == tag1);
-          }
-          if (ok) break;
-          __builtin_amdgcn_s_sleep(1);
-        }
-#pragma unroll
-        for (int i = 0; i < 8; ++i) {
-          int g = t2 * 8 + i;
-          int bb = (g >> 1) & 7, ub = (g >> 4) * 4 + (g & 1) * 2;
-          *(unsigned int*)&w1h[bb][ub] = (unsigned int)e[i];
-        }
-      } else {
-#pragma unroll
-        for (int i = 0; i < 8; ++i) {
-          int g = t2 * 8 + i;
-          int bb = (g >> 1) & 7, ub = (g >> 4) * 4 + (g & 1) * 2;
-          *(unsigned int*)&w1h[bb][ub] = 0u;
-        }
-      }
-    }
-    __syncthreads();
-
-    if (wv == 0) {
-      if (p < 64) {
-        f32x4 acc = {0.f, 0.f, 0.f, 0.f};
-#pragma unroll
-        for (int ch = 0; ch < 8; ++ch) {
-          bf16x8 af = lda_bf8(&v0s[fr][ch * 32 + kg * 8]);
-          acc = __builtin_amdgcn_mfma_f32_16x16x32_bf16(af, frag_of(wfrag[ch]), acc, 0, 0, 0);
-        }
-#pragma unroll
-        for (int j = 0; j < 4; ++j) {
-          int bb2 = (lane >> 4) * 4 + j;
-          if (bb2 < 8) P0[bb2][fr] = acc[j];
-        }
-      }
-    } else if (wv == 1) {
-      if (p >= 1) {
-        f32x4 acc = {0.f, 0.f, 0.f, 0.f};
-#pragma unroll
-        for (int ch = 0; ch < 8; ++ch) {
-          bf16x8 af = lda_bf8(&v0s[fr][ch * 32 + kg * 8]);
-          acc = __builtin_amdgcn_mfma_f32_16x16x32_bf16(af, frag_of(wfrag[ch]), acc, 0, 0, 0);
-        }
-#pragma unroll
-        for (int j = 0; j < 4; ++j) {
-          int bb2 = (lane >> 4) * 4 + j;
-          if (bb2 < 8) P1a[bb2][fr] = acc[j];
-        }
-      }
-    } else if (wv == 2) {
-      if (p >= 1) {
-        f32x4 acc = {0.f, 0.f, 0.f, 0.f};
-#pragma unroll
-        for (int ch = 0; ch < 8; ++ch) {
-          bf16x8 af = lda_bf8(&w1h[fr][ch * 32 + kg * 8]);
-          acc = __builtin_amdgcn_mfma_f32_16x16x32_bf16(af, frag_of(wfrag[ch]), acc, 0, 0, 0);
-        }
-#pragma unroll
-        for (int j = 0; j < 4; ++j) {
-          int bb2 = (lane >> 4) * 4 + j;
-          if (bb2 < 8) P1b[bb2][fr] = acc[j];
-        }
-      }
-    }
-    __syncthreads();
-
-    if (tid < 32 && p < 64) {
-      int b = tid >> 2, uu = tid & 3;
-      float zi = P0[b][uu]      + xz[p][b][uu];
-      float zf = P0[b][4 + uu]  + xz[p][b][4 + uu];
-      float zg = P0[b][8 + uu]  + xz[p][b][8 + uu];
-      float zo = P0[b][12 + uu] + xz[p][b][12 + uu];
-      c0 = sigf(zf) * c0 + sigf(zi) * tanhf(zg);
-      float h = sigf(zo) * tanhf(c0);
-      float hp = __shfl_xor(h, 1);
-      if (!(uu & 1)) {
-        unsigned int d = (unsigned int)f2bf(h) | ((unsigned int)f2bf(hp) << 16);
-        u64 v = ((u64)(unsigned)(p + 1) << 32) | d;
-        __hip_atomic_store(&h0x[(size_t)p * 1024 + blkid * 16 + b * 2 + (uu >> 1)], v,
-                           __ATOMIC_RELAXED, __HIP_MEMORY_SCOPE_AGENT);
-      }
-    } else if (tid >= 32 && tid < 64 && p >= 1) {
-      int t2 = tid - 32, b = t2 >> 2, uu = t2 & 3;
-      float zi = P1a[b][uu]      + P1b[b][uu]      + bias1s[uu];
-      float zf = P1a[b][4 + uu]  + P1b[b][4 + uu]  + bias1s[4 + uu];
-      float zg = P1a[b][8 + uu]  + P1b[b][8 + uu]  + bias1s[8 + uu];
-      float zo = P1a[b][12 + uu] + P1b[b][12 + uu] + bias1s[12 + uu];
-      c1 = sigf(zf) * c1 + sigf(zi) * tanhf(zg);
-      float h = sigf(zo) * tanhf(c1);
-      comb[(size_t)(b * 64 + (p - 1)) * 576 + u0 + uu] = h;
-      float hp = __shfl_xor(h, 1);
-      if (!(uu & 1)) {
-        unsigned int d = (unsigned int)f2bf(h) | ((unsigned int)f2bf(hp) << 16);
-        u64 v = ((u64)(unsigned)p << 32) | d;
-        __hip_atomic_store(&h1x[(size_t)(p - 1) * 1024 + blkid * 16 + b * 2 + (uu >> 1)], v,
-                           __ATOMIC_RELAXED, __HIP_MEMORY_SCOPE_AGENT);
-      }
     }
   }
 }
@@ -734,28 +767,34 @@
   unsigned short* wt2 = (unsigned short*)(ws + base); base += 2304;
   unsigned short* wt3 = (unsigned short*)(ws + base); base += 9216;
   unsigned short* wt4 = (unsigned short*)(ws + base); base += 36864;
+  float* xzg = ws + base; base += 524288;
+  float* cst = ws + base; base += 4096;
 
   prep_wt<<<384, TPB, 0, stream>>>(cw1, cw2, cw3, cw4, wt1, wt2, wt3, wt4);
   permute_fw1<<<512, TPB, 0, stream>>>(fw1, fw1bf);
-
-  conv1_tap<<<4096, TPB, 0, stream>>>(fmap, iseq, wt1, cb1, y1bf, part);
+  hipMemsetAsync(h0x, 0, 2 * 64 * 1024 * sizeof(u64), stream);
+
+  k_conv1<<<NLB + 4096, TPB, 0, stream>>>(fmap, iseq, wt1, cb1, y1bf, part,
+      iseq, mw, mb, w_ih0, w_hh0, b_ih0, b_hh0, w_ih1, w_hh1, b_ih1, b_hh1,
+      h0x, h1x, comb, xzg, cst, 0, 24, 1);
   stats_final3<<<16, TPB, 0, stream>>>(part, g1, be1, ss1, 1.f / 2097152.f, 16, 1, 4096);
-  conv_tap<16, 32, 1, 64, 32><<<8192, TPB, 0, stream>>>(y1bf, ss1, wt2, cb2, y2bf, part);
+  k_conv<16, 32, 1, 64, 32><<<NLB + 8192, TPB, 0, stream>>>(y1bf, ss1, wt2, cb2, y2bf, part,
+      iseq, mw, mb, w_ih0, w_hh0, b_ih0, b_hh0, w_ih1, w_hh1, b_ih1, b_hh1,
+      h0x, h1x, comb, xzg, cst, 24, 38, 0);
   stats_final3<<<32, TPB, 0, stream>>>(part, g2, be2, ss2, 1.f / 524288.f, 32, 1, 8192);
-  conv_tap<32, 64, 1, 32, 16><<<2048, TPB, 0, stream>>>(y2bf, ss2, wt3, cb3, y3bf, part);
+  k_conv<32, 64, 1, 32, 16><<<NLB + 2048, TPB, 0, stream>>>(y2bf, ss2, wt3, cb3, y3bf, part,
+      iseq, mw, mb, w_ih0, w_hh0, b_ih0, b_hh0, w_ih1, w_hh1, b_ih1, b_hh1,
+      h0x, h1x, comb, xzg, cst, 38, 45, 0);
   stats_final3<<<64, TPB, 0, stream>>>(part, g3, be3, ss3, 1.f / 131072.f, 64, 1, 2048);
-  conv_tap<64, 32, 4, 16, 8><<<2048, TPB, 0, stream>>>(y3bf, ss3, wt4, cb4, y4pre, part);
+  k_conv<64, 32, 4, 16, 8><<<NLB + 2048, TPB, 0, stream>>>(y3bf, ss3, wt4, cb4, y4pre, part,
+      iseq, mw, mb, w_ih0, w_hh0, b_ih0, b_hh0, w_ih1, w_hh1, b_ih1, b_hh1,
+      h0x, h1x, comb, xzg, cst, 45, 52, 0);
   stats_final3<<<128, TPB, 0, stream>>>(part, g4, be4, ss4, 1.f / 32768.f, 32, 4, 2048);
-
-  hipMemsetAsync(h0x, 0, 2 * 64 * 1024 * sizeof(u64), stream);
-  lstm_kernel<<<NLB, TPB, 0, stream>>>(iseq, mw, mb,
-                                       w_ih0, w_hh0, b_ih0, b_hh0,
-                                       w_ih1, w_hh1, b_ih1, b_hh1,
-                                       h0x, h1x, comb);
-
-  fc1_mfma<<<dim3(8, 8), TPB, 0, stream>>>(y4pre, fw1bf, ss4, fb1, f1);
+  k_fc1<<<NLB + 64, TPB, 0, stream>>>(y4pre, fw1bf, ss4, fb1, f1,
+      iseq, mw, mb, w_ih0, w_hh0, b_ih0, b_hh0, w_ih1, w_hh1, b_ih1, b_hh1,
+      h0x, h1x, comb, xzg, cst, 52, 65, 0);
+
   gemm_m64<<<dim3(4, 8), TPB, 0, stream>>>(f1, fw2, fb2, comb, 256, 512, 0, 576, 256);
-
   cond_enc<<<8, TPB, 0, stream>>>(cond, steps, ew1, eb1, ew2, eb2, comb);
 
   gemm_m64<<<dim3(2, 8), TPB, 0, stream>>>(comb, xw1, xb1, cx1, 128, 576, 1, 128, 0);
```

After: 592.5 us (median of 2 runs). 1.14x faster.
